# Kernel tuning notes

Hardware: AMD Instinct MI355X
Metric: run time of the kernel (lower is better)

## Reference

```python
import jax, jax.numpy as jnp
import numpy as np

B, S, D, H = 2, 2048, 1024, 16
HD = D // H
NEG = -9000000000000000.0


def setup_inputs() -> dict:
    key = jax.random.key(0)
    ks = jax.random.split(key, 12)
    scale = 1.0 / np.sqrt(D)
    inp = {
        "k": jax.random.normal(ks[0], (B, S, D), jnp.float32),
        "q": jax.random.normal(ks[1], (B, S, D), jnp.float32),
        "v": jax.random.normal(ks[2], (B, S, D), jnp.float32),
        # causal mask, float (0/1), shape [B, 1, S, S] as expected by __call__
        "mask": jnp.broadcast_to(jnp.tril(jnp.ones((S, S), jnp.float32))[None, None], (B, 1, S, S)),
        "Wq": jax.random.normal(ks[3], (D, D), jnp.float32) * scale,
        "bq": jnp.zeros((D,), jnp.float32),
        "Wk": jax.random.normal(ks[4], (D, D), jnp.float32) * scale,
        "bk": jnp.zeros((D,), jnp.float32),
        "Wv": jax.random.normal(ks[5], (D, D), jnp.float32) * scale,
        "bv": jnp.zeros((D,), jnp.float32),
        "Wo": jax.random.normal(ks[6], (D, D), jnp.float32) * scale,
        "bo": jnp.zeros((D,), jnp.float32),
    }
    return inp


def _split_heads(x):
    # [B, S, D] -> [B, H, S, HD]
    return x.reshape(B, S, H, HD).transpose(0, 2, 1, 3)


def reference(k, q, v, mask, Wq, bq, Wk, bk, Wv, bv, Wo, bo):
    keys = _split_heads(k @ Wk + bk)
    queries = _split_heads(q @ Wq + bq)
    values = _split_heads(v @ Wv + bv)
    # scaled dot product with materialized scores (faithful to source)
    logits = jnp.einsum("bhqd,bhkd->bhqk", queries, keys) / np.sqrt(HD)
    logits = jnp.where(mask == 0, NEG, logits)
    attention = jax.nn.softmax(logits, axis=-1)
    out = jnp.einsum("bhqk,bhkd->bhqd", attention, values)
    out = out.transpose(0, 2, 1, 3).reshape(B, S, D)
    o = out @ Wo + bo
    return (o, attention)
```

## Files before the change

### kernel.cpp

```cpp
#include <hip/hip_runtime.h>
#include <stdint.h>

typedef unsigned short u16;
typedef short short8 __attribute__((ext_vector_type(8)));
typedef unsigned short ushort8 __attribute__((ext_vector_type(8)));
typedef unsigned short us4 __attribute__((ext_vector_type(4)));
typedef float f32x4 __attribute__((ext_vector_type(4)));

#define S_LEN 2048
#define D_DIM 1024
#define H_NUM 16
#define HD_DIM 64

__device__ __forceinline__ float bf2f(u16 u) {
  union { uint32_t i; float f; } x; x.i = ((uint32_t)u) << 16; return x.f;
}
__device__ __forceinline__ u16 f2bf(float f) {
  union { float f; uint32_t i; } x; x.f = f;
  uint32_t u = x.i;
  uint32_t r = (u + 0x7fffu + ((u >> 16) & 1u)) >> 16;
  return (u16)r;
}
__device__ __forceinline__ f32x4 mfma16(short8 a, short8 b, f32x4 c) {
  return __builtin_amdgcn_mfma_f32_16x16x32_bf16(a, b, c, 0, 0, 0);
}
__device__ __forceinline__ bool mask_is_f32(const void* mask) {
  return *(const float*)mask == 1.0f;
}
__device__ __forceinline__ void async_cp16(const u16* g, u16* l) {
  __builtin_amdgcn_global_load_lds((const __attribute__((address_space(1))) unsigned int*)g,
                                   (__attribute__((address_space(3))) unsigned int*)l,
                                   16, 0, 0);
}

__global__ __launch_bounds__(256) void prep(const void* __restrict__ q,
                                            const void* __restrict__ k,
                                            const void* __restrict__ v,
                                            const void* __restrict__ w0,
                                            const void* __restrict__ w1,
                                            const void* __restrict__ w2,
                                            const void* __restrict__ w3,
                                            const void* __restrict__ b0,
                                            const void* __restrict__ b1,
                                            const void* __restrict__ b2,
                                            const void* __restrict__ b3,
                                            u16* __restrict__ Cb,
                                            u16* __restrict__ WT,
                                            float* __restrict__ biasF,
                                            const void* __restrict__ mask) {
  __shared__ u16 t[64][65];
  bool isf32 = mask_is_f32(mask);
  int bid = blockIdx.x;
  int tid = threadIdx.x;
  if (bid < 6144) {
    int z = bid >> 11;
    const void* src = (z == 0) ? q : (z == 1) ? k : v;
    size_t i = ((size_t)(bid & 2047) * 256 + tid) * 8;
    u16* dst = Cb + (size_t)z * 4194304;
    if (isf32) {
      const f32x4* p = (const f32x4*)((const float*)src + i);
      f32x4 a = p[0], b = p[1];
      ushort8 o;
#pragma unroll
      for (int j = 0; j < 4; j++) { o[j] = f2bf(a[j]); o[4 + j] = f2bf(b[j]); }
      *(ushort8*)(dst + i) = o;
    } else {
      *(ushort8*)(dst + i) = *(const ushort8*)((const u16*)src + i);
    }
  } else if (bid < 7168) {
    int t2 = bid - 6144;
    int y = t2 >> 8, tile = t2 & 255;
    const void* W = (y == 0) ? w0 : (y == 1) ? w1 : (y == 2) ? w2 : w3;
    u16* out = WT + (size_t)y * 1048576;
    int r0 = (tile >> 4) * 64, c0 = (tile & 15) * 64;
    int rr = tid >> 6, cc = tid & 63;
#pragma unroll
    for (int i = 0; i < 16; i++) {
      int r = i * 4 + rr;
      size_t idx = (size_t)(r0 + r) * 1024 + c0 + cc;
      t[r][cc] = isf32 ? f2bf(((const float*)W)[idx]) : ((const u16*)W)[idx];
    }
    __syncthreads();
#pragma unroll
    for (int i = 0; i < 16; i++) {
      int r = i * 4 + rr;
      out[(size_t)(c0 + r) * 1024 + r0 + cc] = t[cc][r];
    }
  } else {
    int t3 = bid - 7168;
    int y = t3 >> 2;
    const void* b = (y == 0) ? b0 : (y == 1) ? b1 : (y == 2) ? b2 : b3;
    int i = (t3 & 3) * 256 + tid;
    biasF[y * 1024 + i] = isf32 ? ((const float*)b)[i] : bf2f(((const u16*)b)[i]);
  }
}

__device__ __forceinline__ void gemm_body(const u16* __restrict__ A,
                                          const u16* __restrict__ Bt,
                                          const float* __restrict__ bias,
                                          void* __restrict__ C, int mode,
                                          int m0, int n0, u16* lds) {
  const int K = 1024, N = 1024;
  u16* lA = lds;
  u16* lB = lds + 8192;
  int tid = threadIdx.x;
  int lane = tid & 63, w = tid >> 6;
  int wr = w >> 1, wc = w & 1;
  f32x4 acc[4][4] = {};
  const int nk = K >> 5;
  int grow = lane >> 2, gcol = (lane & 3) * 8;

#define GEMM_ISSUE(kt, buf)                                                              \
  {                                                                                      \
    _Pragma("unroll") for (int p = 0; p < 2; p++) {                                      \
      async_cp16(A + (size_t)(m0 + p * 64 + w * 16 + grow) * K + (kt) * 32 + gcol,       \
                 &lA[(buf) * 4096 + p * 2048 + w * 512]);                                \
      async_cp16(Bt + (size_t)(n0 + p * 64 + w * 16 + grow) * K + (kt) * 32 + gcol,      \
                 &lB[(buf) * 4096 + p * 2048 + w * 512]);                                \
    }                                                                                    \
  }

  GEMM_ISSUE(0, 0);
  __syncthreads();
  int cur = 0;
  for (int kt = 0; kt < nk; kt++) {
    if (kt + 1 < nk) GEMM_ISSUE(kt + 1, cur ^ 1);
    short8 af[4], bf[4];
#pragma unroll
    for (int i = 0; i < 4; i++) {
      af[i] = *(const short8*)(&lA[cur * 4096 + (wr * 64 + i * 16 + (lane & 15)) * 32 + (lane >> 4) * 8]);
      bf[i] = *(const short8*)(&lB[cur * 4096 + (wc * 64 + i * 16 + (lane & 15)) * 32 + (lane >> 4) * 8]);
    }
#pragma unroll
    for (int i = 0; i < 4; i++)
#pragma unroll
      for (int j = 0; j < 4; j++)
        acc[i][j] = mfma16(af[i], bf[j], acc[i][j]);
    __syncthreads();
    cur ^= 1;
  }
#undef GEMM_ISSUE
#pragma unroll
  for (int j = 0; j < 4; j++) {
    int col = n0 + wc * 64 + j * 16 + (lane & 15);
    float bv = bias[col];
#pragma unroll
    for (int i = 0; i < 4; i++) {
      int row0 = m0 + wr * 64 + i * 16 + ((lane >> 4) << 2);
      if (mode == 2) {
        int bb = row0 >> 11, s = row0 & 2047;
        int h = col >> 6, hd = col & 63;
        us4 pv;
#pragma unroll
        for (int jj = 0; jj < 4; jj++) pv[jj] = f2bf(acc[i][j][jj] + bv);
        *(us4*)((u16*)C + (((size_t)(bb * 16 + h) * 64 + hd) << 11) + s) = pv;
      } else {
#pragma unroll
        for (int jj = 0; jj < 4; jj++) {
          float val = acc[i][j][jj] + bv;
          if (mode == 1) ((float*)C)[(size_t)(row0 + jj) * N + col] = val;
          else ((u16*)C)[(size_t)(row0 + jj) * N + col] = f2bf(val);
        }
      }
    }
  }
}

__global__ __launch_bounds__(256, 3) void qkv_gemm(const u16* __restrict__ Ab,
                                                   const u16* __restrict__ WTall,
                                                   const float* __restrict__ biasF,
                                                   u16* __restrict__ QKbase,
                                                   u16* __restrict__ Vt) {
  __shared__ __align__(16) u16 smem[16384];
  int z = blockIdx.z;
  void* C = (z == 2) ? (void*)Vt : (void*)(QKbase + (size_t)z * 4194304);
  gemm_body(Ab + (size_t)z * 4194304, WTall + (size_t)z * 1048576, biasF + z * 1024,
            C, (z == 2) ? 2 : 0, blockIdx.y * 128, blockIdx.x * 128, smem);
}

__global__ __launch_bounds__(256, 3) void mid_fused(const u16* __restrict__ Qg,
                                                    const u16* __restrict__ Kg,
                                                    const u16* __restrict__ VtG,
                                                    u16* __restrict__ ctx,
                                                    void* __restrict__ dout,
                                                    const void* __restrict__ mask) {
  __shared__ __align__(16) u16 lK[2][64 * 72];
  __shared__ __align__(16) u16 lV[2][64 * 72];
  __shared__ __align__(16) u16 lP[4][16 * 72];
  bool isf32 = mask_is_f32(mask);
  int bid = blockIdx.x;
  int tid = threadIdx.x, lane = tid & 63, w = tid >> 6;
  int sr = tid >> 3, sc8 = (tid & 7) * 8;

  if (bid < 512) {
    int x = bid & 15, bh = bid >> 4;
    int b = bh >> 4, h = bh & 15;
    u16* lPw = &lP[w][0];
    for (int s = 0; s < 2; s++) {
      int qt = (s == 0) ? x : 31 - x;
      int q0 = qt * 64;
      int nkv = qt + 1;
      int qrow = q0 + w * 16 + (lane & 15);

      short8 qf[2];
#pragma unroll
      for (int ks = 0; ks < 2; ks++)
        qf[ks] = *(const short8*)(Qg + (size_t)(b * S_LEN + qrow) * D_DIM +
                                  h * HD_DIM + ks * 32 + (lane >> 4) * 8);

      ushort8 kreg[2], vreg[2];
      auto loadK = [&](int kt) {
#pragma unroll
        for (int p = 0; p < 2; p++)
          kreg[p] = *(const ushort8*)(Kg + (size_t)(b * S_LEN + kt * 64 + p * 32 + sr) * D_DIM +
                                      h * HD_DIM + sc8);
      };
      auto writeK = [&](int buf) {
#pragma unroll
        for (int p = 0; p < 2; p++)
          *(ushort8*)(&lK[buf][(p * 32 + sr) * 72 + sc8]) = kreg[p];
      };
      auto loadV = [&](int kt) {
#pragma unroll
        for (int p = 0; p < 2; p++)
          vreg[p] = *(const ushort8*)(VtG + (size_t)(bh * HD_DIM + p * 32 + sr) * S_LEN +
                                      kt * 64 + sc8);
      };
      auto writeV = [&](int buf) {
#pragma unroll
        for (int p = 0; p < 2; p++)
          *(ushort8*)(&lV[buf][(p * 32 + sr) * 72 + sc8]) = vreg[p];
      };

      float l_ = 0.f;
      f32x4 oacc[4] = {};

      loadK(0); loadV(0); writeK(0); writeV(0);
      __syncthreads();
      int cur = 0;
      for (int kt = 0; kt < nkv; kt++) {
        if (kt + 1 < nkv) { loadK(kt + 1); loadV(kt + 1); }
        f32x4 sc[4];
#pragma unroll
        for (int j = 0; j < 4; j++) {
          short8 kf0 = *(const short8*)(&lK[cur][(j * 16 + (lane & 15)) * 72 + (lane >> 4) * 8]);
          short8 kf1 = *(const short8*)(&lK[cur][(j * 16 + (lane & 15)) * 72 + 32 + (lane >> 4) * 8]);
          f32x4 a = {0.f, 0.f, 0.f, 0.f};
          a = mfma16(kf0, qf[0], a);
          a = mfma16(kf1, qf[1], a);
          sc[j] = a;
        }
        bool needmask = (kt == qt);
#pragma unroll
        for (int j = 0; j < 4; j++) {
          us4 pb;
#pragma unroll
          for (int jj = 0; jj < 4; jj++) {
            float p = __expf(sc[j][jj] * 0.125f);
            if (needmask) {
              int kv = kt * 64 + j * 16 + ((lane >> 4) << 2) + jj;
              if (kv > qrow) p = 0.f;
            }
            l_ += p;
            pb[jj] = f2bf(p);
          }
          *(us4*)(&lPw[(lane & 15) * 72 + j * 16 + ((lane >> 4) << 2)]) = pb;
        }
        short8 pa[2];
#pragma unroll
        for (int ks = 0; ks < 2; ks++)
          pa[ks] = *(const short8*)(&lPw[(lane & 15) * 72 + ks * 32 + (lane >> 4) * 8]);
#pragma unroll
        for (int f = 0; f < 4; f++) {
          short8 vb0 = *(const short8*)(&lV[cur][(f * 16 + (lane & 15)) * 72 + (lane >> 4) * 8]);
          short8 vb1 = *(const short8*)(&lV[cur][(f * 16 + (lane & 15)) * 72 + 32 + (lane >> 4) * 8]);
          oacc[f] = mfma16(pa[0], vb0, oacc[f]);
          oacc[f] = mfma16(pa[1], vb1, oacc[f]);
        }
        if (kt + 1 < nkv) { writeK(cur ^ 1); writeV(cur ^ 1); }
        __syncthreads();
        cur ^= 1;
      }

      float lr = l_ + __shfl_xor(l_, 16);
      lr += __shfl_xor(lr, 32);
      float invl = 1.f / lr;
      float io[4];
#pragma unroll
      for (int jj = 0; jj < 4; jj++) io[jj] = __shfl(invl, ((lane >> 4) << 2) + jj);
#pragma unroll
      for (int f = 0; f < 4; f++)
#pragma unroll
        for (int jj = 0; jj < 4; jj++) {
          int row = q0 + w * 16 + ((lane >> 4) << 2) + jj;
          int col = h * HD_DIM + f * 16 + (lane & 15);
          ctx[(size_t)(b * S_LEN + row) * D_DIM + col] = f2bf(oacc[f][jj] * io[jj]);
        }
    }
    return;
  }

  int pb = bid - 512;
  int x = pb & 15, bh = pb >> 4;
  int b = bh >> 4, h = bh & 15;
  float* attnF = (float*)dout + 4194304;
  u16* attnB = (u16*)dout + 4194304;

  for (int s = 0; s < 2; s++) {
    int qt = (s == 0) ? x : 31 - x;
    int q0 = qt * 64;
    int nkv = qt + 1;
    int qrow = q0 + w * 16 + (lane & 15);

    short8 qf[2];
#pragma unroll
    for (int ks = 0; ks < 2; ks++)
      qf[ks] = *(const short8*)(Qg + (size_t)(b * S_LEN + qrow) * D_DIM +
                                h * HD_DIM + ks * 32 + (lane >> 4) * 8);

    ushort8 kreg[2];
    auto loadK = [&](int kt) {
#pragma unroll
      for (int p = 0; p < 2; p++)
        kreg[p] = *(const ushort8*)(Kg + (size_t)(b * S_LEN + kt * 64 + p * 32 + sr) * D_DIM +
                                    h * HD_DIM + sc8);
    };
    auto writeK = [&](int buf) {
#pragma unroll
      for (int p = 0; p < 2; p++)
        *(ushort8*)(&lK[buf][(p * 32 + sr) * 72 + sc8]) = kreg[p];
    };

    float l_ = 0.f;
    loadK(0); writeK(0);
    __syncthreads();
    int cur = 0;
    for (int kt = 0; kt < nkv; kt++) {
      if (kt + 1 < nkv) loadK(kt + 1);
      bool needmask = (kt == qt);
#pragma unroll
      for (int j = 0; j < 4; j++) {
        short8 kf0 = *(const short8*)(&lK[cur][(j * 16 + (lane & 15)) * 72 + (lane >> 4) * 8]);
        short8 kf1 = *(const short8*)(&lK[cur][(j * 16 + (lane & 15)) * 72 + 32 + (lane >> 4) * 8]);
        f32x4 a = {0.f, 0.f, 0.f, 0.f};
        a = mfma16(kf0, qf[0], a);
        a = mfma16(kf1, qf[1], a);
#pragma unroll
        for (int jj = 0; jj < 4; jj++) {
          float p = __expf(a[jj] * 0.125f);
          if (needmask) {
            int kv = kt * 64 + j * 16 + ((lane >> 4) << 2) + jj;
            if (kv > qrow) p = 0.f;
          }
          l_ += p;
        }
      }
      if (kt + 1 < nkv) writeK(cur ^ 1);
      __syncthreads();
      cur ^= 1;
    }
    float lr = l_ + __shfl_xor(l_, 16);
    lr += __shfl_xor(lr, 32);
    float invl = 1.f / lr;

    loadK(0); writeK(cur);
    __syncthreads();
    for (int kt = 0; kt < nkv; kt++) {
      if (kt + 1 < nkv) loadK(kt + 1);
      bool needmask = (kt == qt);
#pragma unroll
      for (int j = 0; j < 4; j++) {
        short8 kf0 = *(const short8*)(&lK[cur][(j * 16 + (lane & 15)) * 72 + (lane >> 4) * 8]);
        short8 kf1 = *(const short8*)(&lK[cur][(j * 16 + (lane & 15)) * 72 + 32 + (lane >> 4) * 8]);
        f32x4 a = {0.f, 0.f, 0.f, 0.f};
        a = mfma16(kf0, qf[0], a);
        a = mfma16(kf1, qf[1], a);
        f32x4 p4;
        us4 pbv;
#pragma unroll
        for (int jj = 0; jj < 4; jj++) {
          float p = __expf(a[jj] * 0.125f) * invl;
          if (needmask) {
            int kv = kt * 64 + j * 16 + ((lane >> 4) << 2) + jj;
            if (kv > qrow) p = 0.f;
          }
          p4[jj] = p;
          pbv[jj] = f2bf(p);
        }
        size_t goff = ((size_t)bh * S_LEN + qrow) * S_LEN + kt * 64 + j * 16 + ((lane >> 4) << 2);
        if (isf32) __builtin_nontemporal_store(p4, (f32x4*)(attnF + goff));
        else __builtin_nontemporal_store(pbv, (us4*)(attnB + goff));
      }
      if (kt + 1 < nkv) writeK(cur ^ 1);
      __syncthreads();
      cur ^= 1;
    }

    {
      int z0 = nkv * 64;
      if (isf32) {
        int zc4 = (S_LEN - z0) >> 2;
        if (zc4 > 0) {
          f32x4 zz = {0.f, 0.f, 0.f, 0.f};
          for (int r = tid >> 5; r < 64; r += 8)
            for (int c = tid & 31; c < zc4; c += 32)
              __builtin_nontemporal_store(zz, (f32x4*)(attnF + ((size_t)bh * S_LEN + q0 + r) * S_LEN + z0 + c * 4));
        }
      } else {
        int zc8 = (S_LEN - z0) >> 3;
        if (zc8 > 0) {
          ushort8 zz = {0, 0, 0, 0, 0, 0, 0, 0};
          for (int r = tid >> 5; r < 64; r += 8)
            for (int c = tid & 31; c < zc8; c += 32)
              __builtin_nontemporal_store(zz, (ushort8*)(attnB + ((size_t)bh * S_LEN + q0 + r) * S_LEN + z0 + c * 8));
        }
      }
    }
  }
}

__global__ __launch_bounds__(256, 3) void out_gemm(const u16* __restrict__ ctx,
                                                   const u16* __restrict__ WoT,
                                                   const float* __restrict__ biasO,
                                                   void* __restrict__ dout,
                                                   const void* __restrict__ mask) {
  __shared__ __align__(16) u16 smem[16384];
  bool isf32 = mask_is_f32(mask);
  int bid = blockIdx.x;
  gemm_body(ctx, WoT, biasO, dout, isf32 ? 1 : 0,
            (bid >> 3) * 128, (bid & 7) * 128, smem);
}

extern "C" void kernel_launch(void* const* d_in, const int* in_sizes, int n_in,
                              void* d_out, int out_size, void* d_ws, size_t ws_size,
                              hipStream_t stream) {
  const void* kin = d_in[0];
  const void* qin = d_in[1];
  const void* vin = d_in[2];
  const void* mask = d_in[3];
  const void* Wq = d_in[4];
  const void* bq = d_in[5];
  const void* Wk = d_in[6];
  const void* bk = d_in[7];
  const void* Wv = d_in[8];
  const void* bv = d_in[9];
  const void* Wo = d_in[10];
  const void* bo = d_in[11];

  u16* ws = (u16*)d_ws;
  u16* WT = ws;
  float* biasF = (float*)(ws + 4 * 1048576);
  u16* Cb = ws + 4 * 1048576 + 8192;
  u16* Qp = Cb + 3 * 4194304;
  u16* Kp = Qp + 4194304;
  u16* Vt = Kp + 4194304;
  u16* ctx = Vt + 4194304;

  prep<<<7184, 256, 0, stream>>>(qin, kin, vin, Wq, Wk, Wv, Wo, bq, bk, bv, bo,
                                 Cb, WT, biasF, mask);
  qkv_gemm<<<dim3(8, 32, 3), 256, 0, stream>>>(Cb, WT, biasF, Qp, Vt);
  mid_fused<<<1024, 256, 0, stream>>>(Qp, Kp, Vt, ctx, d_out, mask);
  out_gemm<<<256, 256, 0, stream>>>(ctx, WT + 3 * 1048576, biasF + 3072, d_out, mask);
}
```

Baseline: 259.5 us.

## Merge context PV pass into attention-probability pass's first sweep

Before, separate blocks computed the context (QK^T, softmax, PV) and the attention probabilities (two passes over K). Now one block's first pass over K also loads V and accumulates PV, writing the context, then does the second pass to write normalized probabilities. This drops the duplicated QK^T work and K reads of the old 512 context blocks, but halves the grid to 512 blocks, lowering parallelism and making each block longer.

```diff
diff --git a/kernel.cpp b/kernel.cpp
--- a/kernel.cpp
+++ b/kernel.cpp
@@ -191,118 +191,9 @@
   int bid = blockIdx.x;
   int tid = threadIdx.x, lane = tid & 63, w = tid >> 6;
   int sr = tid >> 3, sc8 = (tid & 7) * 8;
-
-  if (bid < 512) {
-    int x = bid & 15, bh = bid >> 4;
-    int b = bh >> 4, h = bh & 15;
-    u16* lPw = &lP[w][0];
-    for (int s = 0; s < 2; s++) {
-      int qt = (s == 0) ? x : 31 - x;
-      int q0 = qt * 64;
-      int nkv = qt + 1;
-      int qrow = q0 + w * 16 + (lane & 15);
-
-      short8 qf[2];
-#pragma unroll
-      for (int ks = 0; ks < 2; ks++)
-        qf[ks] = *(const short8*)(Qg + (size_t)(b * S_LEN + qrow) * D_DIM +
-                                  h * HD_DIM + ks * 32 + (lane >> 4) * 8);
-
-      ushort8 kreg[2], vreg[2];
-      auto loadK = [&](int kt) {
-#pragma unroll
-        for (int p = 0; p < 2; p++)
-          kreg[p] = *(const ushort8*)(Kg + (size_t)(b * S_LEN + kt * 64 + p * 32 + sr) * D_DIM +
-                                      h * HD_DIM + sc8);
-      };
-      auto writeK = [&](int buf) {
-#pragma unroll
-        for (int p = 0; p < 2; p++)
-          *(ushort8*)(&lK[buf][(p * 32 + sr) * 72 + sc8]) = kreg[p];
-      };
-      auto loadV = [&](int kt) {
-#pragma unroll
-        for (int p = 0; p < 2; p++)
-          vreg[p] = *(const ushort8*)(VtG + (size_t)(bh * HD_DIM + p * 32 + sr) * S_LEN +
-                                      kt * 64 + sc8);
-      };
-      auto writeV = [&](int buf) {
-#pragma unroll
-        for (int p = 0; p < 2; p++)
-          *(ushort8*)(&lV[buf][(p * 32 + sr) * 72 + sc8]) = vreg[p];
-      };
-
-      float l_ = 0.f;
-      f32x4 oacc[4] = {};
-
-      loadK(0); loadV(0); writeK(0); writeV(0);
-      __syncthreads();
-      int cur = 0;
-      for (int kt = 0; kt < nkv; kt++) {
-        if (kt + 1 < nkv) { loadK(kt + 1); loadV(kt + 1); }
-        f32x4 sc[4];
-#pragma unroll
-        for (int j = 0; j < 4; j++) {
-          short8 kf0 = *(const short8*)(&lK[cur][(j * 16 + (lane & 15)) * 72 + (lane >> 4) * 8]);
-          short8 kf1 = *(const short8*)(&lK[cur][(j * 16 + (lane & 15)) * 72 + 32 + (lane >> 4) * 8]);
-          f32x4 a = {0.f, 0.f, 0.f, 0.f};
-          a = mfma16(kf0, qf[0], a);
-          a = mfma16(kf1, qf[1], a);
-          sc[j] = a;
-        }
-        bool needmask = (kt == qt);
-#pragma unroll
-        for (int j = 0; j < 4; j++) {
-          us4 pb;
-#pragma unroll
-          for (int jj = 0; jj < 4; jj++) {
-            float p = __expf(sc[j][jj] * 0.125f);
-            if (needmask) {
-              int kv = kt * 64 + j * 16 + ((lane >> 4) << 2) + jj;
-              if (kv > qrow) p = 0.f;
-            }
-            l_ += p;
-            pb[jj] = f2bf(p);
-          }
-          *(us4*)(&lPw[(lane & 15) * 72 + j * 16 + ((lane >> 4) << 2)]) = pb;
-        }
-        short8 pa[2];
-#pragma unroll
-        for (int ks = 0; ks < 2; ks++)
-          pa[ks] = *(const short8*)(&lPw[(lane & 15) * 72 + ks * 32 + (lane >> 4) * 8]);
-#pragma unroll
-        for (int f = 0; f < 4; f++) {
-          short8 vb0 = *(const short8*)(&lV[cur][(f * 16 + (lane & 15)) * 72 + (lane >> 4) * 8]);
-          short8 vb1 = *(const short8*)(&lV[cur][(f * 16 + (lane & 15)) * 72 + 32 + (lane >> 4) * 8]);
-          oacc[f] = mfma16(pa[0], vb0, oacc[f]);
-          oacc[f] = mfma16(pa[1], vb1, oacc[f]);
-        }
-        if (kt + 1 < nkv) { writeK(cur ^ 1); writeV(cur ^ 1); }
-        __syncthreads();
-        cur ^= 1;
-      }
-
-      float lr = l_ + __shfl_xor(l_, 16);
-      lr += __shfl_xor(lr, 32);
-      float invl = 1.f / lr;
-      float io[4];
-#pragma unroll
-      for (int jj = 0; jj < 4; jj++) io[jj] = __shfl(invl, ((lane >> 4) << 2) + jj);
-#pragma unroll
-      for (int f = 0; f < 4; f++)
-#pragma unroll
-        for (int jj = 0; jj < 4; jj++) {
-          int row = q0 + w * 16 + ((lane >> 4) << 2) + jj;
-          int col = h * HD_DIM + f * 16 + (lane & 15);
-          ctx[(size_t)(b * S_LEN + row) * D_DIM + col] = f2bf(oacc[f][jj] * io[jj]);
-        }
-    }
-    return;
-  }
-
-  int pb = bid - 512;
-  int x = pb & 15, bh = pb >> 4;
+  int x = bid & 15, bh = bid >> 4;
   int b = bh >> 4, h = bh & 15;
+  u16* lPw = &lP[w][0];
   float* attnF = (float*)dout + 4194304;
   u16* attnB = (u16*)dout + 4194304;
 
@@ -318,7 +209,7 @@
       qf[ks] = *(const short8*)(Qg + (size_t)(b * S_LEN + qrow) * D_DIM +
                                 h * HD_DIM + ks * 32 + (lane >> 4) * 8);
 
-    ushort8 kreg[2];
+    ushort8 kreg[2], vreg[2];
     auto loadK = [&](int kt) {
 #pragma unroll
       for (int p = 0; p < 2; p++)
@@ -330,14 +221,26 @@
       for (int p = 0; p < 2; p++)
         *(ushort8*)(&lK[buf][(p * 32 + sr) * 72 + sc8]) = kreg[p];
     };
+    auto loadV = [&](int kt) {
+#pragma unroll
+      for (int p = 0; p < 2; p++)
+        vreg[p] = *(const ushort8*)(VtG + (size_t)(bh * HD_DIM + p * 32 + sr) * S_LEN +
+                                    kt * 64 + sc8);
+    };
+    auto writeV = [&](int buf) {
+#pragma unroll
+      for (int p = 0; p < 2; p++)
+        *(ushort8*)(&lV[buf][(p * 32 + sr) * 72 + sc8]) = vreg[p];
+    };
 
     float l_ = 0.f;
-    loadK(0); writeK(0);
+    f32x4 oacc[4] = {};
+    loadK(0); loadV(0); writeK(0); writeV(0);
     __syncthreads();
     int cur = 0;
     for (int kt = 0; kt < nkv; kt++) {
-      if (kt + 1 < nkv) loadK(kt + 1);
-      bool needmask = (kt == qt);
+      if (kt + 1 < nkv) { loadK(kt + 1); loadV(kt + 1); }
+      f32x4 sc[4];
 #pragma unroll
       for (int j = 0; j < 4; j++) {
         short8 kf0 = *(const short8*)(&lK[cur][(j * 16 + (lane & 15)) * 72 + (lane >> 4) * 8]);
@@ -345,23 +248,54 @@
         f32x4 a = {0.f, 0.f, 0.f, 0.f};
         a = mfma16(kf0, qf[0], a);
         a = mfma16(kf1, qf[1], a);
+        sc[j] = a;
+      }
+      bool needmask = (kt == qt);
+#pragma unroll
+      for (int j = 0; j < 4; j++) {
+        us4 pb;
 #pragma unroll
         for (int jj = 0; jj < 4; jj++) {
-          float p = __expf(a[jj] * 0.125f);
+          float p = __expf(sc[j][jj] * 0.125f);
           if (needmask) {
             int kv = kt * 64 + j * 16 + ((lane >> 4) << 2) + jj;
             if (kv > qrow) p = 0.f;
           }
           l_ += p;
-        }
-      }
-      if (kt + 1 < nkv) writeK(cur ^ 1);
+          pb[jj] = f2bf(p);
+        }
+        *(us4*)(&lPw[(lane & 15) * 72 + j * 16 + ((lane >> 4) << 2)]) = pb;
+      }
+      short8 pa[2];
+#pragma unroll
+      for (int ks = 0; ks < 2; ks++)
+        pa[ks] = *(const short8*)(&lPw[(lane & 15) * 72 + ks * 32 + (lane >> 4) * 8]);
+#pragma unroll
+      for (int f = 0; f < 4; f++) {
+        short8 vb0 = *(const short8*)(&lV[cur][(f * 16 + (lane & 15)) * 72 + (lane >> 4) * 8]);
+        short8 vb1 = *(const short8*)(&lV[cur][(f * 16 + (lane & 15)) * 72 + 32 + (lane >> 4) * 8]);
+        oacc[f] = mfma16(pa[0], vb0, oacc[f]);
+        oacc[f] = mfma16(pa[1], vb1, oacc[f]);
+      }
+      if (kt + 1 < nkv) { writeK(cur ^ 1); writeV(cur ^ 1); }
       __syncthreads();
       cur ^= 1;
     }
+
     float lr = l_ + __shfl_xor(l_, 16);
     lr += __shfl_xor(lr, 32);
     float invl = 1.f / lr;
+    float io[4];
+#pragma unroll
+    for (int jj = 0; jj < 4; jj++) io[jj] = __shfl(invl, ((lane >> 4) << 2) + jj);
+#pragma unroll
+    for (int f = 0; f < 4; f++)
+#pragma unroll
+      for (int jj = 0; jj < 4; jj++) {
+        int row = q0 + w * 16 + ((lane >> 4) << 2) + jj;
+        int col = h * HD_DIM + f * 16 + (lane & 15);
+        ctx[(size_t)(b * S_LEN + row) * D_DIM + col] = f2bf(oacc[f][jj] * io[jj]);
+      }
 
     loadK(0); writeK(cur);
     __syncthreads();
@@ -459,6 +393,6 @@
   prep<<<7184, 256, 0, stream>>>(qin, kin, vin, Wq, Wk, Wv, Wo, bq, bk, bv, bo,
                                  Cb, WT, biasF, mask);
   qkv_gemm<<<dim3(8, 32, 3), 256, 0, stream>>>(Cb, WT, biasF, Qp, Vt);
-  mid_fused<<<1024, 256, 0, stream>>>(Qp, Kp, Vt, ctx, d_out, mask);
+  mid_fused<<<512, 256, 0, stream>>>(Qp, Kp, Vt, ctx, d_out, mask);
   out_gemm<<<256, 256, 0, stream>>>(ctx, WT + 3 * 1048576, biasF + 3072, d_out, mask);
 }
```

Result: faster. 249.8 us (median of 3 runs) (-3.7%).
